# Kernel optimization log

Hardware: AMD Instinct MI355X
Metric: run time of the kernel (lower is better)

The kernel has to match this reference:

```python
import jax, jax.numpy as jnp
import numpy as np

N = 4096     # batch of positions
E = 32       # descriptor buckets (experts)
NBLK = 12    # residual blocks per head


def _ln(x, g, b, eps=1e-5):
    m = x.mean(-1, keepdims=True)
    v = ((x - m) ** 2).mean(-1, keepdims=True)
    return (x - m) / jnp.sqrt(v + eps) * g + b


def _gelu(x):
    return jax.nn.gelu(x, approximate=False)  # torch nn.GELU default = exact erf


def setup_inputs() -> dict:
    key = jax.random.key(0)
    ks = iter(jax.random.split(key, 64))

    def nrm(shape, scale=0.05):
        return jax.random.normal(next(ks), shape, jnp.float32) * scale

    return {
        "piece_idx": jax.random.randint(next(ks), (N, 64), 0, 12),
        "side_flag": jax.random.randint(next(ks), (N,), 0, 2),
        "ep_file": jax.random.randint(next(ks), (N,), 0, 8),
        "castle_ms": jax.random.uniform(next(ks), (N, 4), jnp.float32),
        "fifty_a": jax.random.uniform(next(ks), (N,), jnp.float32),
        "descriptor_index": jax.random.randint(next(ks), (N,), 0, E),
        # per-bucket embedding tables, stacked on a leading expert axis
        "Wp_w": nrm((E, 64, 12, 32)), "Wp_b": nrm((E, 64, 12, 32)),
        "Wc_w": nrm((E, 4, 32)), "Wc_b": nrm((E, 4, 32)),
        "Wep_w": nrm((E, 8, 32)), "Wep_b": nrm((E, 8, 32)),
        "Wf_w": nrm((E, 2, 32)), "Wf_b": nrm((E, 2, 32)),
        # per-bucket MLP head params (weights stored as [in,out])
        "fc1_w": nrm((E, 2240, 256)), "fc1_b": nrm((E, 256)),
        "ln1_g": jnp.ones((E, 256)), "ln1_b": jnp.zeros((E, 256)),
        "fc2_w": nrm((E, 256, 32)), "fc2_b": nrm((E, 32)),
        "ln2_g": jnp.ones((E, 32)), "ln2_b": jnp.zeros((E, 32)),
        "blkA_w": nrm((NBLK, E, 32, 32)), "blkA_b": nrm((NBLK, E, 32)),
        "blkA_g": jnp.ones((NBLK, E, 32)), "blkA_be": jnp.zeros((NBLK, E, 32)),
        "blkB_w": nrm((NBLK, E, 32, 32)), "blkB_b": nrm((NBLK, E, 32)),
        "blkB_g": jnp.ones((NBLK, E, 32)), "blkB_be": jnp.zeros((NBLK, E, 32)),
        "out_w": nrm((E, 32, 51)), "out_b": nrm((E, 51)),
        "bins": jnp.linspace(0.0, 1.0, 51),
    }


def reference(piece_idx, side_flag, ep_file, castle_ms, fifty_a, descriptor_index,
              Wp_w, Wp_b, Wc_w, Wc_b, Wep_w, Wep_b, Wf_w, Wf_b,
              fc1_w, fc1_b, ln1_g, ln1_b, fc2_w, fc2_b, ln2_g, ln2_b,
              blkA_w, blkA_b, blkA_g, blkA_be, blkB_w, blkB_b, blkB_g, blkB_be,
              out_w, out_b, bins):
    desc = descriptor_index
    side = side_flag.astype(bool)
    n = piece_idx.shape[0]

    # ---- per-bucket, side-selected embedding gathers -> x_emb [N,2240] ----
    sq = jnp.arange(64)
    pc = jnp.maximum(piece_idx, 0)                                 # clamp -1 -> 0
    w_emb = Wp_w[desc[:, None], sq[None, :], pc]                    # [N,64,32]
    b_emb = Wp_b[desc[:, None], sq[None, :], pc]
    piece_emb = jnp.where(side[:, None, None], b_emb, w_emb)
    piece_emb = piece_emb * (piece_idx >= 0)[..., None].astype(piece_emb.dtype)
    pieces_vec = piece_emb.reshape(n, 2048)

    Wc = jnp.where(side[:, None, None], Wc_b[desc], Wc_w[desc])     # [N,4,32]
    castle_vec = (castle_ms[..., None] * Wc).reshape(n, 128)

    Wep = jnp.where(side[:, None, None], Wep_b[desc], Wep_w[desc])  # [N,8,32]
    epc = jnp.maximum(ep_file, 0)
    ep_vec = jnp.take_along_axis(Wep, epc[:, None, None], axis=1)[:, 0]
    ep_vec = ep_vec * (ep_file >= 0)[:, None].astype(ep_vec.dtype)

    Wf = jnp.where(side[:, None, None], Wf_b[desc], Wf_w[desc])     # [N,2,32]
    fifty_vec = (1.0 - fifty_a)[:, None] * Wf[:, 0] + fifty_a[:, None] * Wf[:, 1]

    x = jnp.concatenate([pieces_vec, castle_vec, ep_vec, fifty_vec], axis=1)  # [N,2240]

    # ---- expert-routed dense layer: all-expert GEMM + per-token select ----
    def dense_moe(h, W, b):
        ha = jnp.einsum('nd,edh->neh', h, W)                        # [N,E,out]
        hsel = jnp.take_along_axis(ha, desc[:, None, None], axis=1)[:, 0]
        return hsel + b[desc]

    h = _ln(_gelu(dense_moe(x, fc1_w, fc1_b)), ln1_g[desc], ln1_b[desc])   # [N,256]
    h = _ln(_gelu(dense_moe(h, fc2_w, fc2_b)), ln2_g[desc], ln2_b[desc])   # [N,32]

    def blk(carry, p):
        wA, bA, gA, beA, wB, bB, gB, beB = p
        y = _ln(_gelu(dense_moe(carry, wA, bA)), gA[desc], beA[desc])
        y = _ln(_gelu(dense_moe(y, wB, bB)), gB[desc], beB[desc])
        return carry + y, None

    h, _ = jax.lax.scan(blk, h, (blkA_w, blkA_b, blkA_g, blkA_be,
                                 blkB_w, blkB_b, blkB_g, blkB_be))

    logits = dense_moe(_gelu(h), out_w, out_b)                      # [N,51]
    p_win = jnp.sum(jax.nn.softmax(logits, axis=-1) * bins, axis=-1, keepdims=True)
    return logits, p_win
```

## Files before the change

kernel.cpp:

```cpp
#include <hip/hip_runtime.h>
#include <math.h>

#define N 4096
#define E 32
#define NBLK 12
#define D_IN 2240
#define H1 256
#define H2 32
#define NOUT 51
#define MT 16
#define NPAD (N + E*(MT-1))
#define NTILE (NPAD/MT)
#define KSPLIT 8
#define NROWS 4608
#define GMAX 96

typedef short s8v __attribute__((ext_vector_type(8)));
typedef float f4v __attribute__((ext_vector_type(4)));

__device__ __forceinline__ float gelu(float x){
    return 0.5f * x * (1.0f + erff(x * 0.70710678118654752f));
}
__device__ __forceinline__ unsigned short f2bf(float f){
    unsigned int u = __float_as_uint(f);
    unsigned int r = (u + 0x7fffu + ((u >> 16) & 1u)) >> 16;
    return (unsigned short)r;
}
__device__ __forceinline__ float bflo(unsigned int u){ return __uint_as_float(u << 16); }
__device__ __forceinline__ float bfhi(unsigned int u){ return __uint_as_float(u & 0xffff0000u); }

template<int CTRL>
__device__ __forceinline__ float dppadd(float x){
    int y = __builtin_amdgcn_update_dpp(0, __float_as_int(x), CTRL, 0xF, 0xF, true);
    return x + __int_as_float(y);
}
__device__ __forceinline__ float red32(float x){
    x = dppadd<0x121>(x);
    x = dppadd<0x122>(x);
    x = dppadd<0x124>(x);
    x = dppadd<0x128>(x);
    int y = __builtin_amdgcn_ds_swizzle(__float_as_int(x), 0x401F);
    return x + __int_as_float(y);
}

__global__ void k_pack(const float* __restrict__ W2,
                       const float* __restrict__ Aw, const float* __restrict__ Bw,
                       unsigned int* __restrict__ w2pk_g, unsigned int* __restrict__ rpk_g){
    int j = blockIdx.x*256 + threadIdx.x;
    if (j < E*4096){
        int e = j >> 12, idx = j & 4095;
        int h = idx & 1, q = idx >> 1, cc = q & 31, p2 = q >> 5;
        int k0 = 4*p2 + 2*h;
        const float* W2e = W2 + (size_t)e*H1*H2;
        unsigned int lo = f2bf(W2e[k0*32 + cc]);
        unsigned int hi = f2bf(W2e[(k0+1)*32 + cc]);
        w2pk_g[((size_t)e << 12) + (p2*32 + cc)*2 + h] = lo | (hi << 16);
    } else {
        int i = j - E*4096;
        int slot = i & 511;
        int m = i >> 9;
        int e = m & 31, mat = m >> 5;
        int tb = mat >> 1, s = mat & 1;
        int h = slot & 1, q = slot >> 1, cc = q & 31, p2 = q >> 5;
        int k0 = 4*p2 + 2*h;
        const float* src = s ? Bw : Aw;
        size_t base = ((size_t)tb*E + e)*1024;
        unsigned int lo = f2bf(src[base + k0*32 + cc]);
        unsigned int hi = f2bf(src[base + (k0+1)*32 + cc]);
        rpk_g[((size_t)m << 9) + slot] = lo | (hi << 16);
    }
}

__global__ void k_prep(const int* __restrict__ piece_idx,
                       const int* __restrict__ side_flag,
                       const int* __restrict__ ep_file,
                       const float* __restrict__ castle_ms,
                       const float* __restrict__ fifty_a,
                       const int* __restrict__ desc_idx,
                       const float* __restrict__ Wp_w, const float* __restrict__ Wp_b,
                       const float* __restrict__ Wc_w, const float* __restrict__ Wc_b,
                       const float* __restrict__ Wep_w, const float* __restrict__ Wep_b,
                       const float* __restrict__ Wf_w, const float* __restrict__ Wf_b,
                       unsigned short* __restrict__ xs,
                       int* __restrict__ perm, int* __restrict__ tile_e,
                       int4* __restrict__ garr, int* __restrict__ ngroups){
    int tid = threadIdx.x;
    if (blockIdx.x == 0){
        __shared__ int scnt[E];
        __shared__ int spoff[E+1];
        __shared__ int scur[E];
        if (tid < E) scnt[tid] = 0;
        __syncthreads();
        for (int n = tid; n < N; n += blockDim.x) atomicAdd(&scnt[desc_idx[n]], 1);
        __syncthreads();
        if (tid == 0){
            int run = 0;
            for (int e = 0; e < E; e++){ spoff[e] = run; run += ((scnt[e] + MT - 1)/MT)*MT; }
            spoff[E] = run;
            int ng = 0;
            for (int e = 0; e < E; e++){
                int t0 = spoff[e]/MT, t1 = spoff[e+1]/MT;
                for (int t = t0; t < t1; t += 8){
                    int nv = t1 - t; if (nv > 8) nv = 8;
                    if (ng < GMAX) garr[ng] = make_int4(t, e, nv, 0);
                    ng++;
                }
            }
            *ngroups = (ng > GMAX) ? GMAX : ng;
        }
        __syncthreads();
        if (tid < E) scur[tid] = spoff[tid];
        for (int p = tid; p < NPAD + 64; p += blockDim.x) perm[p] = -1;
        __syncthreads();
        for (int n = tid; n < N; n += blockDim.x){
            int p = atomicAdd(&scur[desc_idx[n]], 1);
            perm[p] = n;
        }
        for (int t = tid; t < NTILE; t += blockDim.x){
            int p0 = t*MT;
            int e = -1;
            if (p0 < spoff[E]){
                for (int q = 0; q < E; q++){
                    if (p0 >= spoff[q] && p0 < spoff[q+1]){ e = q; break; }
                }
            }
            tile_e[t] = e;
        }
        s8v z = {0,0,0,0,0,0,0,0};
        for (int i = tid; i < D_IN/8; i += blockDim.x)
            *(s8v*)(xs + (size_t)N*D_IN + i*8) = z;
        return;
    }
    int row = blockIdx.x - 1;
    unsigned short* xr = xs + (size_t)row * D_IN;
    int d = desc_idx[row];
    int s = side_flag[row];
    __shared__ int pidx[64];
    if (tid < 64) pidx[tid] = piece_idx[row*64 + tid];
    __syncthreads();
    const float* Wp  = s ? Wp_b  : Wp_w;
    const float* Wc  = s ? Wc_b  : Wc_w;
    const float* Wep = s ? Wep_b : Wep_w;
    const float* Wf  = s ? Wf_b  : Wf_w;
    int ep  = ep_file[row];
    int epc = ep > 0 ? ep : 0;
    float a = fifty_a[row];
    for (int t = tid; t < D_IN/8; t += blockDim.x){
        int i0 = t*8;
        float v[8];
        if (i0 < 2048){
            int sq = i0 >> 5, c0 = i0 & 31;
            int pc = pidx[sq];
            float msk = pc >= 0 ? 1.0f : 0.0f;
            int pcc = pc > 0 ? pc : 0;
            const float* base = Wp + (((size_t)d*64 + sq)*12 + pcc)*32 + c0;
            float4 a0 = *(const float4*)base;
            float4 a1 = *(const float4*)(base + 4);
            v[0]=a0.x*msk; v[1]=a0.y*msk; v[2]=a0.z*msk; v[3]=a0.w*msk;
            v[4]=a1.x*msk; v[5]=a1.y*msk; v[6]=a1.z*msk; v[7]=a1.w*msk;
        } else if (i0 < 2176){
            int j = i0 - 2048; int ci = j >> 5, c0 = j & 31;
            float cv = castle_ms[row*4 + ci];
            const float* base = Wc + ((size_t)d*4 + ci)*32 + c0;
            float4 a0 = *(const float4*)base;
            float4 a1 = *(const float4*)(base + 4);
            v[0]=a0.x*cv; v[1]=a0.y*cv; v[2]=a0.z*cv; v[3]=a0.w*cv;
            v[4]=a1.x*cv; v[5]=a1.y*cv; v[6]=a1.z*cv; v[7]=a1.w*cv;
        } else if (i0 < 2208){
            int c0 = i0 - 2176;
            float msk = ep >= 0 ? 1.0f : 0.0f;
            const float* base = Wep + ((size_t)d*8 + epc)*32 + c0;
            float4 a0 = *(const float4*)base;
            float4 a1 = *(const float4*)(base + 4);
            v[0]=a0.x*msk; v[1]=a0.y*msk; v[2]=a0.z*msk; v[3]=a0.w*msk;
            v[4]=a1.x*msk; v[5]=a1.y*msk; v[6]=a1.z*msk; v[7]=a1.w*msk;
        } else {
            int c0 = i0 - 2208;
            #pragma unroll
            for (int j = 0; j < 8; j++)
                v[j] = (1.0f - a) * Wf[(size_t)d*64 + c0 + j] + a * Wf[(size_t)d*64 + 32 + c0 + j];
        }
        s8v p;
        #pragma unroll
        for (int j = 0; j < 8; j++) p[j] = (short)f2bf(v[j]);
        *(s8v*)(xr + i0) = p;
    }
}

__launch_bounds__(256)
__global__ void k_fc1(const int4* __restrict__ garr, const int* __restrict__ ngroups,
                      const unsigned short* __restrict__ xs,
                      const int* __restrict__ perm,
                      const float* __restrict__ W1,
                      float* __restrict__ h1p){
    int g = blockIdx.x;
    if (g >= *ngroups) return;
    int4 gi = garr[g];
    int tile0 = gi.x, e = gi.y, nv = gi.z;
    int kc = blockIdx.y, nh = blockIdx.z;
    int kstart = (kc < 6) ? kc*9 : 54 + (kc-6)*8;
    int nsteps = (kc < 6) ? 9 : 8;
    int tid = threadIdx.x;
    int lane = tid & 63, wave = tid >> 6;
    int quad = lane >> 4, l16 = lane & 15;

    const unsigned short* Arow[8];
    #pragma unroll
    for (int mt = 0; mt < 8; mt++){
        int p = perm[(tile0 + mt)*MT + l16];
        if (p < 0) p = N;
        Arow[mt] = xs + (size_t)p*D_IN + quad*8;
    }

    const float* Bp = W1 + (size_t)e*D_IN*H1 + nh*128;
    int cl0 = wave*32 + l16;
    int cl1 = cl0 + 16;

    f4v acc[8][2];
    #pragma unroll
    for (int mt = 0; mt < 8; mt++){ acc[mt][0] = (f4v){0.f,0.f,0.f,0.f}; acc[mt][1] = (f4v){0.f,0.f,0.f,0.f}; }

    int kend = kstart + nsteps;
    for (int s = kstart; s < kend; s++){
        int kb = s*32;
        int krow = kb + quad*8;
        float b0f[8], b1f[8];
        #pragma unroll
        for (int j = 0; j < 8; j++){
            b0f[j] = Bp[(size_t)(krow + j)*H1 + cl0];
            b1f[j] = Bp[(size_t)(krow + j)*H1 + cl1];
        }
        s8v b0, b1;
        #pragma unroll
        for (int j = 0; j < 8; j++){
            b0[j] = (short)f2bf(b0f[j]);
            b1[j] = (short)f2bf(b1f[j]);
        }
        #pragma unroll
        for (int mt = 0; mt < 8; mt++){
            s8v av = *(const s8v*)(Arow[mt] + kb);
            acc[mt][0] = __builtin_amdgcn_mfma_f32_16x16x32_bf16(av, b0, acc[mt][0], 0, 0, 0);
            acc[mt][1] = __builtin_amdgcn_mfma_f32_16x16x32_bf16(av, b1, acc[mt][1], 0, 0, 0);
        }
    }
    int col0 = nh*128 + wave*32 + l16;
    float* out = h1p + (size_t)kc*NROWS*H1;
    #pragma unroll
    for (int mt = 0; mt < 8; mt++){
        if (mt >= nv) break;
        int posb = (tile0 + mt)*MT + quad*4;
        #pragma unroll
        for (int r = 0; r < 4; r++){
            out[(size_t)(posb + r)*H1 + col0]      = acc[mt][0][r];
            out[(size_t)(posb + r)*H1 + col0 + 16] = acc[mt][1][r];
        }
    }
}

__launch_bounds__(256)
__global__ void k_tail(const int* __restrict__ tile_e, const int* __restrict__ perm,
                       const float* __restrict__ h1p, const float* __restrict__ b1,
                       const float* __restrict__ g1, const float* __restrict__ be1,
                       const unsigned int* __restrict__ w2pk_g, const float* __restrict__ b2,
                       const float* __restrict__ g2, const float* __restrict__ be2,
                       const unsigned int* __restrict__ rpk,
                       const float* __restrict__ Abv, const float* __restrict__ Ag,
                       const float* __restrict__ Abe,
                       const float* __restrict__ Bb, const float* __restrict__ Bg,
                       const float* __restrict__ Bbe,
                       const float* __restrict__ Ow, const float* __restrict__ Ob,
                       const float* __restrict__ bins,
                       float* __restrict__ out){
    int th = blockIdx.x;
    int t  = th >> 1;
    int r0 = (th & 1) * 8;
    int e = tile_e[t];
    if (e < 0) return;
    int tid = threadIdx.x;

    __shared__ __align__(16) float        shf[8*260];
    __shared__ __align__(16) unsigned int W2pk[4096];
    __shared__ __align__(16) float        vecs[NBLK*6*32];
    __shared__ __align__(16) float        sh2[8][36];
    __shared__ __align__(16) float        sh3[8][36];

    {
        const unsigned int* src = w2pk_g + ((size_t)e << 12);
        for (int j = tid; j < 4096; j += 256) W2pk[j] = src[j];
    }
    for (int j = tid; j < NBLK*6*32; j += 256){
        int cc = j & 31, vi = (j >> 5) % 6, tb = j / 192;
        size_t wb = (size_t)tb*E + e;
        const float* src;
        switch(vi){ case 0: src=Abv; break; case 1: src=Ag; break; case 2: src=Abe; break;
                    case 3: src=Bb;  break; case 4: src=Bg; break; default: src=Bbe; }
        vecs[j] = src[wb*32 + cc];
    }
    #pragma unroll
    for (int it = 0; it < 2; it++){
        int slot = it*256 + tid;
        int r = slot >> 6, c4 = (slot & 63) << 2;
        int row = t*MT + r0 + r;
        float4 v = {0.f,0.f,0.f,0.f};
        #pragma unroll
        for (int kc = 0; kc < KSPLIT; kc++){
            float4 p = *(const float4*)(h1p + ((size_t)kc*NROWS + row)*H1 + c4);
            v.x += p.x; v.y += p.y; v.z += p.z; v.w += p.w;
        }
        float4 bb = *(const float4*)(b1 + e*H1 + c4);
        shf[r*260 + c4]   = gelu(v.x + bb.x);
        shf[r*260 + c4+1] = gelu(v.y + bb.y);
        shf[r*260 + c4+2] = gelu(v.z + bb.z);
        shf[r*260 + c4+3] = gelu(v.w + bb.w);
    }
    __syncthreads();

    int m = tid >> 5, c = tid & 31;
    {
        float s = 0.f, s2 = 0.f;
        #pragma unroll
        for (int j = 0; j < 8; j++){
            float x = shf[m*260 + c + 32*j];
            s += x; s2 += x*x;
        }
        s  = red32(s);
        s2 = red32(s2);
        float mean = s * (1.0f/H1);
        float var  = s2 * (1.0f/H1) - mean*mean;
        float rs = rsqrtf(var + 1e-5f);
        #pragma unroll
        for (int j = 0; j < 8; j++){
            int k = c + 32*j;
            shf[m*260 + k] = (shf[m*260 + k] - mean) * rs * g1[e*H1 + k] + be1[e*H1 + k];
        }
    }
    float hv;
    {
        const uint2* W2p = (const uint2*)W2pk;
        float q0=0.f,q1=0.f,q2=0.f,q3=0.f;
        #pragma unroll 8
        for (int p2 = 0; p2 < 64; p2++){
            uint2 w = W2p[p2*32 + c];
            float4 h4 = *(const float4*)(shf + m*260 + p2*4);
            q0 = fmaf(h4.x, bflo(w.x), q0);
            q1 = fmaf(h4.y, bfhi(w.x), q1);
            q2 = fmaf(h4.z, bflo(w.y), q2);
            q3 = fmaf(h4.w, bfhi(w.y), q3);
        }
        float acc = (q0+q1) + (q2+q3) + b2[e*H2 + c];
        float y = gelu(acc);
        float s  = red32(y);
        float s2 = red32(y*y);
        float mean2 = s * (1.0f/H2);
        float var2  = s2 * (1.0f/H2) - mean2*mean2;
        hv = (y - mean2) * rsqrtf(var2 + 1e-5f) * g2[e*H2+c] + be2[e*H2+c];
    }

    for (int tb = 0; tb < NBLK; tb++){
        const float* vA = &vecs[tb*192];
        const uint2* WA = (const uint2*)(rpk + (((size_t)(tb*2+0)*E + e) << 9));
        const uint2* WB = (const uint2*)(rpk + (((size_t)(tb*2+1)*E + e) << 9));
        sh2[m][c] = hv;
        float q0=0.f,q1=0.f,q2=0.f,q3=0.f;
        #pragma unroll
        for (int p2 = 0; p2 < 8; p2++){
            uint2 w = WA[p2*32 + c];
            float4 h4 = *(const float4*)(&sh2[m][p2*4]);
            q0 = fmaf(h4.x, bflo(w.x), q0);
            q1 = fmaf(h4.y, bfhi(w.x), q1);
            q2 = fmaf(h4.z, bflo(w.y), q2);
            q3 = fmaf(h4.w, bfhi(w.y), q3);
        }
        float ya = (q0+q1) + (q2+q3) + vA[c];
        ya = gelu(ya);
        float sa  = red32(ya);
        float sa2 = red32(ya*ya);
        float ma = sa * (1.0f/H2);
        float va = sa2 * (1.0f/H2) - ma*ma;
        float yA = (ya - ma) * rsqrtf(va + 1e-5f) * vA[32+c] + vA[64+c];
        sh3[m][c] = yA;
        q0=0.f; q1=0.f; q2=0.f; q3=0.f;
        #pragma unroll
        for (int p2 = 0; p2 < 8; p2++){
            uint2 w = WB[p2*32 + c];
            float4 h4 = *(const float4*)(&sh3[m][p2*4]);
            q0 = fmaf(h4.x, bflo(w.x), q0);
            q1 = fmaf(h4.y, bfhi(w.x), q1);
            q2 = fmaf(h4.z, bflo(w.y), q2);
            q3 = fmaf(h4.w, bfhi(w.y), q3);
        }
        float yb = (q0+q1) + (q2+q3) + vA[96+c];
        yb = gelu(yb);
        float sb  = red32(yb);
        float sb2 = red32(yb*yb);
        float mb = sb * (1.0f/H2);
        float vb = sb2 * (1.0f/H2) - mb*mb;
        hv += (yb - mb) * rsqrtf(vb + 1e-5f) * vA[128+c] + vA[160+c];
    }

    sh2[m][c] = gelu(hv);
    __syncthreads();
    int wave = tid >> 6, lane = tid & 63;
    const float* W = Ow + (size_t)e*32*NOUT;
    for (int rr = wave; rr < 8; rr += 4){
        int orow = perm[t*MT + r0 + rr];
        if (orow < 0) continue;
        float acc = (lane < NOUT) ? Ob[e*NOUT + lane] : -INFINITY;
        #pragma unroll
        for (int k = 0; k < 32; k++){
            float gk = sh2[rr][k];
            if (lane < NOUT) acc = fmaf(gk, W[k*NOUT + lane], acc);
        }
        if (lane < NOUT) out[(size_t)orow*NOUT + lane] = acc;
        float mx = acc;
        #pragma unroll
        for (int o = 32; o > 0; o >>= 1) mx = fmaxf(mx, __shfl_xor(mx, o));
        float pp = (lane < NOUT) ? expf(acc - mx) : 0.0f;
        float sum = pp;
        float pb = (lane < NOUT) ? pp * bins[lane] : 0.0f;
        float sb = pb;
        #pragma unroll
        for (int o = 32; o > 0; o >>= 1){ sum += __shfl_xor(sum, o); sb += __shfl_xor(sb, o); }
        if (lane == 0) out[(size_t)N*NOUT + orow] = sb / sum;
    }
}

extern "C" void kernel_launch(void* const* d_in, const int* in_sizes, int n_in,
                              void* d_out, int out_size, void* d_ws, size_t ws_size,
                              hipStream_t stream){
    const int*   piece_idx = (const int*)d_in[0];
    const int*   side_flag = (const int*)d_in[1];
    const int*   ep_file   = (const int*)d_in[2];
    const float* castle_ms = (const float*)d_in[3];
    const float* fifty_a   = (const float*)d_in[4];
    const int*   desc      = (const int*)d_in[5];
    const float* Wp_w  = (const float*)d_in[6];
    const float* Wp_b  = (const float*)d_in[7];
    const float* Wc_w  = (const float*)d_in[8];
    const float* Wc_b  = (const float*)d_in[9];
    const float* Wep_w = (const float*)d_in[10];
    const float* Wep_b = (const float*)d_in[11];
    const float* Wf_w  = (const float*)d_in[12];
    const float* Wf_b  = (const float*)d_in[13];
    const float* fc1_w = (const float*)d_in[14];
    const float* fc1_b = (const float*)d_in[15];
    const float* ln1_g = (const float*)d_in[16];
    const float* ln1_b = (const float*)d_in[17];
    const float* fc2_w = (const float*)d_in[18];
    const float* fc2_b = (const float*)d_in[19];
    const float* ln2_g = (const float*)d_in[20];
    const float* ln2_b = (const float*)d_in[21];
    const float* blkA_w  = (const float*)d_in[22];
    const float* blkA_b  = (const float*)d_in[23];
    const float* blkA_g  = (const float*)d_in[24];
    const float* blkA_be = (const float*)d_in[25];
    const float* blkB_w  = (const float*)d_in[26];
    const float* blkB_b  = (const float*)d_in[27];
    const float* blkB_g  = (const float*)d_in[28];
    const float* blkB_be = (const float*)d_in[29];
    const float* out_w = (const float*)d_in[30];
    const float* out_b = (const float*)d_in[31];
    const float* bins  = (const float*)d_in[32];

    char* wsp = (char*)d_ws;
    auto alloc = [&](size_t bytes){ void* p = (void*)wsp; wsp += (bytes + 255) & ~(size_t)255; return p; };
    int*            perm    = (int*)            alloc((size_t)(NPAD+128)*4);
    int*            tile_e  = (int*)            alloc((size_t)NTILE*4);
    int4*           garr    = (int4*)           alloc((size_t)GMAX*16);
    int*            ngroups = (int*)            alloc(256);
    unsigned int*   w2pk_g  = (unsigned int*)   alloc((size_t)E*4096*4);
    unsigned int*   rpk     = (unsigned int*)   alloc((size_t)24*E*512*4);
    unsigned short* xs      = (unsigned short*) alloc((size_t)(N+128)*D_IN*2);
    float*          h1p     = (float*)          alloc((size_t)KSPLIT*NROWS*H1*4);

    k_pack<<<2048, 256, 0, stream>>>(fc2_w, blkA_w, blkB_w, w2pk_g, rpk);
    k_prep<<<1 + N, 256, 0, stream>>>(piece_idx, side_flag, ep_file,
                                      castle_ms, fifty_a, desc,
                                      Wp_w, Wp_b, Wc_w, Wc_b,
                                      Wep_w, Wep_b, Wf_w, Wf_b,
                                      xs, perm, tile_e, garr, ngroups);
    k_fc1<<<dim3(GMAX, KSPLIT, 2), 256, 0, stream>>>(garr, ngroups, xs, perm, fc1_w, h1p);
    k_tail<<<NTILE*2, 256, 0, stream>>>(tile_e, perm, h1p, fc1_b, ln1_g, ln1_b,
                                        w2pk_g, fc2_b, ln2_g, ln2_b,
                                        rpk,
                                        blkA_b, blkA_g, blkA_be,
                                        blkB_b, blkB_g, blkB_be,
                                        out_w, out_b, bins, (float*)d_out);
}
```

Measured before the change: 294.8 us.

## Write bf16 activations in expert-sorted order so fc1 reads contiguous rows

The routing/permutation computation moves from k_prep's first block into an extra block of k_pack. k_prep then builds each activation row directly at its sorted, padded position, writing zeros for padding slots. k_fc1 can therefore read contiguous tile rows without a perm gather, which should improve load coalescing and drop the indirection. The cost is that k_prep now launches NPAD blocks instead of N+1 and writes a larger xs buffer.

```diff
diff --git a/kernel.cpp b/kernel.cpp
--- a/kernel.cpp
+++ b/kernel.cpp
@@ -45,8 +45,55 @@
 
 __global__ void k_pack(const float* __restrict__ W2,
                        const float* __restrict__ Aw, const float* __restrict__ Bw,
-                       unsigned int* __restrict__ w2pk_g, unsigned int* __restrict__ rpk_g){
-    int j = blockIdx.x*256 + threadIdx.x;
+                       const int* __restrict__ desc_idx,
+                       unsigned int* __restrict__ w2pk_g, unsigned int* __restrict__ rpk_g,
+                       int* __restrict__ perm, int* __restrict__ tile_e,
+                       int4* __restrict__ garr, int* __restrict__ ngroups){
+    int tid = threadIdx.x;
+    if (blockIdx.x == 2048){
+        __shared__ int scnt[E];
+        __shared__ int spoff[E+1];
+        __shared__ int scur[E];
+        if (tid < E) scnt[tid] = 0;
+        __syncthreads();
+        for (int n = tid; n < N; n += blockDim.x) atomicAdd(&scnt[desc_idx[n]], 1);
+        __syncthreads();
+        if (tid == 0){
+            int run = 0;
+            for (int e = 0; e < E; e++){ spoff[e] = run; run += ((scnt[e] + MT - 1)/MT)*MT; }
+            spoff[E] = run;
+            int ng = 0;
+            for (int e = 0; e < E; e++){
+                int t0 = spoff[e]/MT, t1 = spoff[e+1]/MT;
+                for (int t = t0; t < t1; t += 8){
+                    int nv = t1 - t; if (nv > 8) nv = 8;
+                    if (ng < GMAX) garr[ng] = make_int4(t, e, nv, 0);
+                    ng++;
+                }
+            }
+            *ngroups = (ng > GMAX) ? GMAX : ng;
+        }
+        __syncthreads();
+        if (tid < E) scur[tid] = spoff[tid];
+        for (int p = tid; p < NPAD + 64; p += blockDim.x) perm[p] = -1;
+        __syncthreads();
+        for (int n = tid; n < N; n += blockDim.x){
+            int p = atomicAdd(&scur[desc_idx[n]], 1);
+            perm[p] = n;
+        }
+        for (int t = tid; t < NTILE; t += blockDim.x){
+            int p0 = t*MT;
+            int e = -1;
+            if (p0 < spoff[E]){
+                for (int q = 0; q < E; q++){
+                    if (p0 >= spoff[q] && p0 < spoff[q+1]){ e = q; break; }
+                }
+            }
+            tile_e[t] = e;
+        }
+        return;
+    }
+    int j = blockIdx.x*256 + tid;
     if (j < E*4096){
         int e = j >> 12, idx = j & 4095;
         int h = idx & 1, q = idx >> 1, cc = q & 31, p2 = q >> 5;
@@ -71,7 +118,8 @@
     }
 }
 
-__global__ void k_prep(const int* __restrict__ piece_idx,
+__global__ void k_prep(const int* __restrict__ perm,
+                       const int* __restrict__ piece_idx,
                        const int* __restrict__ side_flag,
                        const int* __restrict__ ep_file,
                        const float* __restrict__ castle_ms,
@@ -81,58 +129,16 @@
                        const float* __restrict__ Wc_w, const float* __restrict__ Wc_b,
                        const float* __restrict__ Wep_w, const float* __restrict__ Wep_b,
                        const float* __restrict__ Wf_w, const float* __restrict__ Wf_b,
-                       unsigned short* __restrict__ xs,
-                       int* __restrict__ perm, int* __restrict__ tile_e,
-                       int4* __restrict__ garr, int* __restrict__ ngroups){
+                       unsigned short* __restrict__ xs){
     int tid = threadIdx.x;
-    if (blockIdx.x == 0){
-        __shared__ int scnt[E];
-        __shared__ int spoff[E+1];
-        __shared__ int scur[E];
-        if (tid < E) scnt[tid] = 0;
-        __syncthreads();
-        for (int n = tid; n < N; n += blockDim.x) atomicAdd(&scnt[desc_idx[n]], 1);
-        __syncthreads();
-        if (tid == 0){
-            int run = 0;
-            for (int e = 0; e < E; e++){ spoff[e] = run; run += ((scnt[e] + MT - 1)/MT)*MT; }
-            spoff[E] = run;
-            int ng = 0;
-            for (int e = 0; e < E; e++){
-                int t0 = spoff[e]/MT, t1 = spoff[e+1]/MT;
-                for (int t = t0; t < t1; t += 8){
-                    int nv = t1 - t; if (nv > 8) nv = 8;
-                    if (ng < GMAX) garr[ng] = make_int4(t, e, nv, 0);
-                    ng++;
-                }
-            }
-            *ngroups = (ng > GMAX) ? GMAX : ng;
-        }
-        __syncthreads();
-        if (tid < E) scur[tid] = spoff[tid];
-        for (int p = tid; p < NPAD + 64; p += blockDim.x) perm[p] = -1;
-        __syncthreads();
-        for (int n = tid; n < N; n += blockDim.x){
-            int p = atomicAdd(&scur[desc_idx[n]], 1);
-            perm[p] = n;
-        }
-        for (int t = tid; t < NTILE; t += blockDim.x){
-            int p0 = t*MT;
-            int e = -1;
-            if (p0 < spoff[E]){
-                for (int q = 0; q < E; q++){
-                    if (p0 >= spoff[q] && p0 < spoff[q+1]){ e = q; break; }
-                }
-            }
-            tile_e[t] = e;
-        }
+    int pos = blockIdx.x;
+    int row = perm[pos];
+    unsigned short* xr = xs + (size_t)pos * D_IN;
+    if (row < 0){
         s8v z = {0,0,0,0,0,0,0,0};
-        for (int i = tid; i < D_IN/8; i += blockDim.x)
-            *(s8v*)(xs + (size_t)N*D_IN + i*8) = z;
+        for (int t = tid; t < D_IN/8; t += blockDim.x) *(s8v*)(xr + t*8) = z;
         return;
     }
-    int row = blockIdx.x - 1;
-    unsigned short* xr = xs + (size_t)row * D_IN;
     int d = desc_idx[row];
     int s = side_flag[row];
     __shared__ int pidx[64];
@@ -190,7 +196,6 @@
 __launch_bounds__(256)
 __global__ void k_fc1(const int4* __restrict__ garr, const int* __restrict__ ngroups,
                       const unsigned short* __restrict__ xs,
-                      const int* __restrict__ perm,
                       const float* __restrict__ W1,
                       float* __restrict__ h1p){
     int g = blockIdx.x;
@@ -204,13 +209,7 @@
     int lane = tid & 63, wave = tid >> 6;
     int quad = lane >> 4, l16 = lane & 15;
 
-    const unsigned short* Arow[8];
-    #pragma unroll
-    for (int mt = 0; mt < 8; mt++){
-        int p = perm[(tile0 + mt)*MT + l16];
-        if (p < 0) p = N;
-        Arow[mt] = xs + (size_t)p*D_IN + quad*8;
-    }
+    const unsigned short* Ab = xs + (size_t)(tile0*MT + l16)*D_IN + quad*8;
 
     const float* Bp = W1 + (size_t)e*D_IN*H1 + nh*128;
     int cl0 = wave*32 + l16;
@@ -238,7 +237,7 @@
         }
         #pragma unroll
         for (int mt = 0; mt < 8; mt++){
-            s8v av = *(const s8v*)(Arow[mt] + kb);
+            s8v av = *(const s8v*)(Ab + (size_t)mt*MT*D_IN + kb);
             acc[mt][0] = __builtin_amdgcn_mfma_f32_16x16x32_bf16(av, b0, acc[mt][0], 0, 0, 0);
             acc[mt][1] = __builtin_amdgcn_mfma_f32_16x16x32_bf16(av, b1, acc[mt][1], 0, 0, 0);
         }
@@ -470,16 +469,16 @@
     int*            ngroups = (int*)            alloc(256);
     unsigned int*   w2pk_g  = (unsigned int*)   alloc((size_t)E*4096*4);
     unsigned int*   rpk     = (unsigned int*)   alloc((size_t)24*E*512*4);
-    unsigned short* xs      = (unsigned short*) alloc((size_t)(N+128)*D_IN*2);
+    unsigned short* xs      = (unsigned short*) alloc((size_t)(NPAD+128)*D_IN*2);
     float*          h1p     = (float*)          alloc((size_t)KSPLIT*NROWS*H1*4);
 
-    k_pack<<<2048, 256, 0, stream>>>(fc2_w, blkA_w, blkB_w, w2pk_g, rpk);
-    k_prep<<<1 + N, 256, 0, stream>>>(piece_idx, side_flag, ep_file,
-                                      castle_ms, fifty_a, desc,
-                                      Wp_w, Wp_b, Wc_w, Wc_b,
-                                      Wep_w, Wep_b, Wf_w, Wf_b,
-                                      xs, perm, tile_e, garr, ngroups);
-    k_fc1<<<dim3(GMAX, KSPLIT, 2), 256, 0, stream>>>(garr, ngroups, xs, perm, fc1_w, h1p);
+    k_pack<<<2049, 256, 0, stream>>>(fc2_w, blkA_w, blkB_w, desc,
+                                     w2pk_g, rpk, perm, tile_e, garr, ngroups);
+    k_prep<<<NPAD, 256, 0, stream>>>(perm, piece_idx, side_flag, ep_file,
+                                     castle_ms, fifty_a, desc,
+                                     Wp_w, Wp_b, Wc_w, Wc_b,
+                                     Wep_w, Wep_b, Wf_w, Wf_b, xs);
+    k_fc1<<<dim3(GMAX, KSPLIT, 2), 256, 0, stream>>>(garr, ngroups, xs, fc1_w, h1p);
     k_tail<<<NTILE*2, 256, 0, stream>>>(tile_e, perm, h1p, fc1_b, ln1_g, ln1_b,
                                         w2pk_g, fc2_b, ln2_g, ln2_b,
                                         rpk,
```

Measured after the change: 296.6 us. Within noise of the previous version (+0.6%).
